# Kernel optimization log

Measured on AMD Instinct MI355X. Metric: run time of the kernel, lower is better.

## Reference

```python
import jax, jax.numpy as jnp
import numpy as np
import math

B, S, D, H = 8, 1024, 512, 8
DH = D // H
SCALE_BASE = 512


def _xpos(x, downscale):
    # x: [B, H, S, DH]; xpos rotary with exponential scale (jamie-stirling RetNet impl)
    s = x.shape[-2]
    d = x.shape[-1]
    half = d // 2
    sv = (jnp.arange(0, d, 2, dtype=jnp.float32) + 0.4 * d) / (1.4 * d)      # [half]
    power = jnp.arange(s, dtype=jnp.float32) / SCALE_BASE
    scale = sv[None, :] ** power[:, None]                                     # [s, half]
    inv_freq = 1.0 / (10000.0 ** (jnp.arange(half, dtype=jnp.float32) / half))
    ang = jnp.arange(s, dtype=jnp.float32)[:, None] * inv_freq[None, :]       # [s, half]
    if downscale:
        scale = 1.0 / scale
    sin = jnp.repeat(jnp.sin(ang) * scale, 2, axis=-1)                        # [s, d]
    cos = jnp.repeat(jnp.cos(ang) * scale, 2, axis=-1)
    rot = jnp.stack((-x[..., 1::2], x[..., ::2]), axis=-1).reshape(x.shape)   # rotate_every_two
    return x * cos + rot * sin


def setup_inputs() -> dict:
    key = jax.random.key(0)
    ks = jax.random.split(key, 7)
    X = jax.random.normal(ks[0], (B, S, D), dtype=jnp.float32)
    # per-head projections stacked: torch init randn/hidden_size
    W_Q = jax.random.normal(ks[1], (H, D, DH), dtype=jnp.float32) / D
    W_K = jax.random.normal(ks[2], (H, D, DH), dtype=jnp.float32) / D
    W_V = jax.random.normal(ks[3], (H, D, DH), dtype=jnp.float32) / D
    W_G = jax.random.normal(ks[4], (D, D), dtype=jnp.float32) / D
    W_O = jax.random.normal(ks[5], (D, D), dtype=jnp.float32) / D
    gn_weight = jnp.ones((D,), dtype=jnp.float32)
    gn_bias = jnp.zeros((D,), dtype=jnp.float32)
    return {"X": X, "W_Q": W_Q, "W_K": W_K, "W_V": W_V, "W_G": W_G,
            "W_O": W_O, "gn_weight": gn_weight, "gn_bias": gn_bias}


def reference(X, W_Q, W_K, W_V, W_G, W_O, gn_weight, gn_bias):
    b, s, _ = X.shape
    # per-head decay gammas and symmetric (non-causal) decay matrix D
    gammas = 1.0 - jnp.exp(jnp.linspace(math.log(1.0 / 32), math.log(1.0 / 512), H)).astype(jnp.float32)
    n = jnp.arange(s)
    Dmat = gammas[:, None, None] ** jnp.abs(n[:, None] - n[None, :]).astype(jnp.float32)  # [H,s,s]
    Q = _xpos(jnp.einsum('bsd,hde->bhse', X, W_Q), False)
    K = _xpos(jnp.einsum('bsd,hde->bhse', X, W_K), True)
    V = jnp.einsum('bsd,hde->bhse', X, W_V)
    scores = jnp.einsum('bhse,bhte->bhst', Q, K)
    p = jax.nn.softmax(scores, axis=-1) * Dmat[None]          # decay-weighted softmax
    Y = jnp.einsum('bhst,bhte->bhse', p, V)                    # [b,H,s,DH]
    Y = jnp.moveaxis(Y, 1, 2).reshape(b, s, H * DH)            # concat heads -> [b,s,D]
    # GroupNorm(H groups) over flattened rows [b*s, D]
    Yg = Y.reshape(-1, H, DH)
    mu = Yg.mean(axis=-1, keepdims=True)
    var = Yg.var(axis=-1, keepdims=True)
    Yn = ((Yg - mu) * jax.lax.rsqrt(var + 1e-5)).reshape(-1, H * DH)
    Yn = (Yn * gn_weight + gn_bias).reshape(b, s, H * DH)
    G = X @ W_G
    swish = G * jax.nn.sigmoid(G)
    return (swish * Yn) @ W_O
```

## Files before the change

### kernel.cpp

```cpp
#include <hip/hip_runtime.h>
#include <math.h>

#define B_ 8
#define S_ 1024
#define D_ 512
#define H_ 8
#define DH_ 64
#define M_ (B_*S_)

typedef __attribute__((ext_vector_type(8))) short short8;
typedef __attribute__((ext_vector_type(4))) short s16x4;
typedef __attribute__((ext_vector_type(4))) float f32x4;

__device__ inline unsigned short bf16h(float x) {
  unsigned u = __float_as_uint(x);
  return (unsigned short)((u + 0x7FFFu + ((u >> 16) & 1u)) >> 16);
}
__device__ inline void tsplit(float x, short& hs, short& ls) {
  unsigned u = __float_as_uint(x);
  hs = (short)(u >> 16);
  float r = x - __uint_as_float(u & 0xFFFF0000u);
  ls = (short)(__float_as_uint(r) >> 16);
}
__device__ inline f32x4 mfma16(short8 a, short8 b, f32x4 c) {
  return __builtin_amdgcn_mfma_f32_16x16x32_bf16(a, b, c, 0, 0, 0);
}

__global__ void xpos_table_kernel(float* __restrict__ tab) {
  int idx = blockIdx.x * 256 + threadIdx.x;
  int s = idx >> 5, i = idx & 31;
  float sv = (2.0f * (float)i + 0.4f * 64.0f) / (1.4f * 64.0f);
  float p = (float)s / 512.0f;
  float scale = powf(sv, p);
  float inv_freq = powf(10000.0f, -((float)i / 32.0f));
  float ang = (float)s * inv_freq;
  float sn = sinf(ang), cs = cosf(ang);
  tab[idx]          = cs * scale;
  tab[32768 + idx]  = sn * scale;
  tab[65536 + idx]  = cs / scale;
  tab[98304 + idx]  = sn / scale;
}

__global__ __launch_bounds__(256) void wprep_kernel(
    const float* __restrict__ Wq, const float* __restrict__ Wk,
    const float* __restrict__ Wv, const float* __restrict__ Wg,
    short* __restrict__ BTh, short* __restrict__ BTl, int gonly) {
  __shared__ float t[64][65];
  const int n0 = blockIdx.x * 64, k0 = blockIdx.y * 64;
  const int tid = threadIdx.x;
  const float* src;
  int ld;
  if (gonly) {
    src = Wg + (size_t)k0 * 512 + n0; ld = 512;
  } else {
    int w = n0 >> 9, nn = n0 & 511;
    if (w == 3) { src = Wg + (size_t)k0 * 512 + nn; ld = 512; }
    else {
      const float* W = (w == 0) ? Wq : ((w == 1) ? Wk : Wv);
      int h = nn >> 6;
      src = W + (size_t)h * D_ * DH_ + (size_t)k0 * 64; ld = 64;
    }
  }
#pragma unroll
  for (int i = 0; i < 4; ++i) {
    int idx = tid + i * 256;
    int kk = idx >> 4, nl4 = (idx & 15) * 4;
    float4 v = *(const float4*)(src + (size_t)kk * ld + nl4);
    t[kk][nl4] = v.x; t[kk][nl4 + 1] = v.y; t[kk][nl4 + 2] = v.z; t[kk][nl4 + 3] = v.w;
  }
  __syncthreads();
#pragma unroll
  for (int i = 0; i < 2; ++i) {
    int idx = tid + i * 256;
    int nl = idx >> 3, ck = idx & 7;
    short8 hh, ll;
#pragma unroll
    for (int j = 0; j < 8; ++j) {
      short h_, l_;
      tsplit(t[ck * 8 + j][nl], h_, l_);
      hh[j] = h_; ll[j] = l_;
    }
    size_t off = (size_t)(n0 + nl) * 512 + k0 + ck * 8;
    *(short8*)(BTh + off) = hh;
    *(short8*)(BTl + off) = ll;
  }
}

template<bool PRESPLIT>
__global__ __launch_bounds__(256) void gemm_mfma_kernel(
    const float* __restrict__ Af,
    const short* __restrict__ Ah, const short* __restrict__ Al,
    const short* __restrict__ BTh, const short* __restrict__ BTl,
    const float* __restrict__ tab,
    short* __restrict__ QhO, short* __restrict__ QlO,
    short* __restrict__ KhO, short* __restrict__ KlO,
    short* __restrict__ VhT, short* __restrict__ VlT,
    float* __restrict__ G, int fused) {
  __shared__ __align__(16) short AsH[128][40];
  __shared__ __align__(16) short AsL[128][40];
  __shared__ __align__(16) short BsH[128][40];
  __shared__ __align__(16) short BsL[128][40];
  const int m0 = blockIdx.x * 128, by = blockIdx.y, n0 = by * 128;
  const int tid = threadIdx.x, w = tid >> 6, lane = tid & 63;
  const int lx = lane & 15, quad = lane >> 4;
  const int wr = w >> 1, wc = w & 1;
  f32x4 acc[4][4] = {};
  for (int k0 = 0; k0 < 512; k0 += 32) {
    if constexpr (PRESPLIT) {
#pragma unroll
      for (int i = 0; i < 2; ++i) {
        int idx = tid + i * 256;
        int r = idx >> 2, sg = (idx & 3) * 8;
        *(short8*)&AsH[r][sg] = *(const short8*)(Ah + (size_t)(m0 + r) * 512 + k0 + sg);
        *(short8*)&AsL[r][sg] = *(const short8*)(Al + (size_t)(m0 + r) * 512 + k0 + sg);
      }
    } else {
      int r = tid >> 1, kh = (tid & 1) * 16;
      const float* ap = Af + (size_t)(m0 + r) * 512 + k0 + kh;
#pragma unroll
      for (int j4 = 0; j4 < 4; ++j4) {
        float4 v = *(const float4*)(ap + j4 * 4);
        s16x4 hh, ll;
        short h_, l_;
        tsplit(v.x, h_, l_); hh[0] = h_; ll[0] = l_;
        tsplit(v.y, h_, l_); hh[1] = h_; ll[1] = l_;
        tsplit(v.z, h_, l_); hh[2] = h_; ll[2] = l_;
        tsplit(v.w, h_, l_); hh[3] = h_; ll[3] = l_;
        *(s16x4*)&AsH[r][kh + j4 * 4] = hh;
        *(s16x4*)&AsL[r][kh + j4 * 4] = ll;
      }
    }
#pragma unroll
    for (int i = 0; i < 2; ++i) {
      int idx = tid + i * 256;
      int r = idx >> 2, sg = (idx & 3) * 8;
      *(short8*)&BsH[r][sg] = *(const short8*)(BTh + (size_t)(n0 + r) * 512 + k0 + sg);
      *(short8*)&BsL[r][sg] = *(const short8*)(BTl + (size_t)(n0 + r) * 512 + k0 + sg);
    }
    __syncthreads();
    short8 fah[4], fal[4], fbh[4], fbl[4];
#pragma unroll
    for (int i = 0; i < 4; ++i) {
      fah[i] = *(const short8*)&AsH[wr * 64 + i * 16 + lx][quad * 8];
      fal[i] = *(const short8*)&AsL[wr * 64 + i * 16 + lx][quad * 8];
      fbh[i] = *(const short8*)&BsH[wc * 64 + i * 16 + lx][quad * 8];
      fbl[i] = *(const short8*)&BsL[wc * 64 + i * 16 + lx][quad * 8];
    }
#pragma unroll
    for (int ms = 0; ms < 4; ++ms)
#pragma unroll
      for (int ns = 0; ns < 4; ++ns) {
        f32x4 a = acc[ms][ns];
        a = mfma16(fah[ms], fbh[ns], a);
        a = mfma16(fal[ms], fbh[ns], a);
        a = mfma16(fah[ms], fbl[ns], a);
        acc[ms][ns] = a;
      }
    __syncthreads();
  }
  if (fused) {
    const int w4 = by >> 2;
    const int ncb = (by & 3) * 128 + wc * 64;
    if (w4 < 2) {
      short* Ph = (w4 == 0) ? QhO : KhO;
      short* Pl = (w4 == 0) ? QlO : KlO;
      const float* ct = tab + (w4 ? 65536 : 0);
      const float* st = tab + (w4 ? 98304 : 32768);
#pragma unroll
      for (int ms = 0; ms < 4; ++ms) {
        const int m = m0 + wr * 64 + ms * 16 + quad * 4;
        const int b = m >> 10, sbase = m & 1023;
#pragma unroll
        for (int ns = 0; ns < 4; ++ns) {
          const int n = ncb + ns * 16 + lx;
          const int h = n >> 6, e = n & 63;
          const int i0 = e >> 1;
          const float sgn = (e & 1) ? 1.0f : -1.0f;
          short* ph = Ph + (((size_t)(b * 8 + h)) * 1024 + sbase) * 64 + e;
          short* pl = Pl + (((size_t)(b * 8 + h)) * 1024 + sbase) * 64 + e;
#pragma unroll
          for (int rg = 0; rg < 4; ++rg) {
            const int s = sbase + rg;
            float v = acc[ms][ns][rg];
            float vp = __shfl_xor(v, 1);
            float o = v * ct[s * 32 + i0] + sgn * vp * st[s * 32 + i0];
            short h_, l_;
            tsplit(o, h_, l_);
            ph[rg * 64] = h_;
            pl[rg * 64] = l_;
          }
        }
      }
    } else if (w4 == 2) {
#pragma unroll
      for (int ms = 0; ms < 4; ++ms) {
        const int m = m0 + wr * 64 + ms * 16 + quad * 4;
        const int b = m >> 10, s = m & 1023;
#pragma unroll
        for (int ns = 0; ns < 4; ++ns) {
          const int n = ncb + ns * 16 + lx;
          const int h = n >> 6, e = n & 63;
          s16x4 hh, ll;
#pragma unroll
          for (int rg = 0; rg < 4; ++rg) {
            short h_, l_;
            tsplit(acc[ms][ns][rg], h_, l_);
            hh[rg] = h_; ll[rg] = l_;
          }
          size_t off = (((size_t)(b * 8 + h)) * 64 + e) * 1024 + s;
          *(s16x4*)(VhT + off) = hh;
          *(s16x4*)(VlT + off) = ll;
        }
      }
    } else {
#pragma unroll
      for (int ms = 0; ms < 4; ++ms) {
        const int m = m0 + wr * 64 + ms * 16 + quad * 4;
#pragma unroll
        for (int ns = 0; ns < 4; ++ns) {
          const int n = ncb + ns * 16 + lx;
#pragma unroll
          for (int rg = 0; rg < 4; ++rg) G[(size_t)(m + rg) * 512 + n] = acc[ms][ns][rg];
        }
      }
    }
  } else {
#pragma unroll
    for (int ms = 0; ms < 4; ++ms) {
      const int m = m0 + wr * 64 + ms * 16 + quad * 4;
#pragma unroll
      for (int ns = 0; ns < 4; ++ns) {
        const int n = n0 + wc * 64 + ns * 16 + lx;
#pragma unroll
        for (int rg = 0; rg < 4; ++rg) G[(size_t)(m + rg) * 512 + n] = acc[ms][ns][rg];
      }
    }
  }
}

__global__ __launch_bounds__(256, 2) void attn_mfma_kernel(
    const short* __restrict__ Qh, const short* __restrict__ Ql,
    const short* __restrict__ Kh, const short* __restrict__ Kl,
    const short* __restrict__ VhT, const short* __restrict__ VlT,
    float* __restrict__ Y) {
  __shared__ __align__(16) short KhS[64][72];
  __shared__ __align__(16) short KlS[64][72];
  __shared__ __align__(16) short VhS[64][72];
  __shared__ __align__(16) short VlS[64][72];
  __shared__ __align__(16) short PhS[4][32][72];
  const int bh = blockIdx.x, s0 = blockIdx.y * 128;
  const int b = bh >> 3, h = bh & 7;
  const int tid = threadIdx.x;
  const int w = tid >> 6, lane = tid & 63;
  const int lx = lane & 15, quad = lane >> 4;
  const int s0w = s0 + w * 32;
  const float l0c = -3.4657359027997265f;
  const float l1c = -6.2383246250395075f;
  const float gamma = 1.0f - expf(l0c + (float)h * (l1c - l0c) / 7.0f);
  const float lg2g = log2f(gamma);
  const short* Qbh = Qh + (size_t)bh * S_ * DH_;
  const short* Qbl = Ql + (size_t)bh * S_ * DH_;
  const short* Kbh = Kh + (size_t)bh * S_ * DH_;
  const short* Kbl = Kl + (size_t)bh * S_ * DH_;
  const short* VbH = VhT + (size_t)bh * DH_ * S_;
  const short* VbL = VlT + (size_t)bh * DH_ * S_;

  float cl[4], cr[4];
#pragma unroll
  for (int ns = 0; ns < 4; ++ns) {
    cl[ns] = exp2f(lg2g * (float)(ns * 16 + lx));
    cr[ns] = exp2f(lg2g * (float)(63 - ns * 16 - lx));
  }

  short8 qfh[2][2], qfl[2][2];
#pragma unroll
  for (int ms = 0; ms < 2; ++ms)
#pragma unroll
    for (int kc = 0; kc < 2; ++kc) {
      size_t off = (size_t)(s0w + ms * 16 + lx) * DH_ + kc * 32 + quad * 8;
      qfh[ms][kc] = *(const short8*)(Qbh + off);
      qfl[ms][kc] = *(const short8*)(Qbl + off);
    }

  f32x4 O[2][4] = {};
  float lsum[2][4] = {};

  for (int t0 = 0; t0 < S_; t0 += 64) {
    __syncthreads();
#pragma unroll
    for (int i = 0; i < 2; ++i) {
      int slot = tid + i * 256;
      int r = slot >> 3, c8 = (slot & 7) * 8;
      *(short8*)&KhS[r][c8] = *(const short8*)(Kbh + (size_t)(t0 + r) * DH_ + c8);
      *(short8*)&KlS[r][c8] = *(const short8*)(Kbl + (size_t)(t0 + r) * DH_ + c8);
      *(short8*)&VhS[r][c8] = *(const short8*)(VbH + (size_t)r * S_ + t0 + c8);
      *(short8*)&VlS[r][c8] = *(const short8*)(VbL + (size_t)r * S_ + t0 + c8);
    }
    __syncthreads();
    f32x4 acc[2][4];
#pragma unroll
    for (int ns = 0; ns < 4; ++ns) {
      short8 kh0 = *(const short8*)&KhS[ns * 16 + lx][quad * 8];
      short8 kh1 = *(const short8*)&KhS[ns * 16 + lx][32 + quad * 8];
      short8 kl0 = *(const short8*)&KlS[ns * 16 + lx][quad * 8];
      short8 kl1 = *(const short8*)&KlS[ns * 16 + lx][32 + quad * 8];
#pragma unroll
      for (int ms = 0; ms < 2; ++ms) {
        f32x4 a = {};
        a = mfma16(qfh[ms][0], kh0, a);
        a = mfma16(qfl[ms][0], kh0, a);
        a = mfma16(qfh[ms][0], kl0, a);
        a = mfma16(qfh[ms][1], kh1, a);
        a = mfma16(qfl[ms][1], kh1, a);
        a = mfma16(qfh[ms][1], kl1, a);
        acc[ms][ns] = a;
      }
    }
    const int cse = (t0 + 63 < s0w) ? 0 : ((t0 > s0w + 31) ? 1 : 2);
#pragma unroll
    for (int ms = 0; ms < 2; ++ms)
#pragma unroll
      for (int rg = 0; rg < 4; ++rg) {
        const int rloc = ms * 16 + quad * 4 + rg;
        const int srow = s0w + rloc;
        float pe[4], p[4];
#pragma unroll
        for (int ns = 0; ns < 4; ++ns) pe[ns] = __expf(acc[ms][ns][rg]);
        lsum[ms][rg] += (pe[0] + pe[1]) + (pe[2] + pe[3]);
        if (cse == 0) {
          float rf = exp2f(lg2g * (float)(srow - t0 - 63));
#pragma unroll
          for (int ns = 0; ns < 4; ++ns) p[ns] = pe[ns] * rf * cr[ns];
        } else if (cse == 1) {
          float rf = exp2f(lg2g * (float)(t0 - srow));
#pragma unroll
          for (int ns = 0; ns < 4; ++ns) p[ns] = pe[ns] * rf * cl[ns];
        } else {
#pragma unroll
          for (int ns = 0; ns < 4; ++ns)
            p[ns] = pe[ns] * exp2f(lg2g * fabsf((float)(srow - (t0 + ns * 16 + lx))));
        }
#pragma unroll
        for (int ns = 0; ns < 4; ++ns)
          PhS[w][rloc][ns * 16 + lx] = (short)bf16h(p[ns]);
      }
    short8 pf[2][2];
#pragma unroll
    for (int ms = 0; ms < 2; ++ms)
#pragma unroll
      for (int kc = 0; kc < 2; ++kc)
        pf[ms][kc] = *(const short8*)&PhS[w][ms * 16 + lx][kc * 32 + quad * 8];
#pragma unroll
    for (int ns = 0; ns < 4; ++ns) {
      short8 vh0 = *(const short8*)&VhS[ns * 16 + lx][quad * 8];
      short8 vh1 = *(const short8*)&VhS[ns * 16 + lx][32 + quad * 8];
      short8 vl0 = *(const short8*)&VlS[ns * 16 + lx][quad * 8];
      short8 vl1 = *(const short8*)&VlS[ns * 16 + lx][32 + quad * 8];
#pragma unroll
      for (int ms = 0; ms < 2; ++ms) {
        f32x4 o = O[ms][ns];
        o = mfma16(pf[ms][0], vh0, o);
        o = mfma16(pf[ms][0], vl0, o);
        o = mfma16(pf[ms][1], vh1, o);
        o = mfma16(pf[ms][1], vl1, o);
        O[ms][ns] = o;
      }
    }
  }
#pragma unroll
  for (int ms = 0; ms < 2; ++ms)
#pragma unroll
    for (int rg = 0; rg < 4; ++rg) {
      float s = lsum[ms][rg];
      s += __shfl_xor(s, 1);
      s += __shfl_xor(s, 2);
      s += __shfl_xor(s, 4);
      s += __shfl_xor(s, 8);
      const float inv = 1.0f / s;
      const int srow = s0w + ms * 16 + quad * 4 + rg;
#pragma unroll
      for (int ns = 0; ns < 4; ++ns)
        Y[((size_t)(b * S_ + srow)) * D_ + h * DH_ + ns * 16 + lx] = O[ms][ns][rg] * inv;
    }
}

__global__ __launch_bounds__(256) void gn_gate_kernel(const float* __restrict__ Y,
                                                      const float* __restrict__ G,
                                                      const float* __restrict__ gnw,
                                                      const float* __restrict__ gnb,
                                                      short* __restrict__ Zh,
                                                      short* __restrict__ Zl) {
  const int r0 = blockIdx.x * 64, h = blockIdx.y, d0 = h * DH_;
  const int tid = threadIdx.x, tx = tid & 15, tyq = tid >> 4;
  float4 wv = *(const float4*)(gnw + d0 + tx * 4);
  float4 bv = *(const float4*)(gnb + d0 + tx * 4);
  float w4[4] = {wv.x, wv.y, wv.z, wv.w};
  float b4[4] = {bv.x, bv.y, bv.z, bv.w};
#pragma unroll
  for (int i = 0; i < 4; ++i) {
    int r = r0 + tyq + i * 16;
    float4 yv = *(const float4*)(Y + (size_t)r * D_ + d0 + tx * 4);
    float y[4] = {yv.x, yv.y, yv.z, yv.w};
    float s = y[0] + y[1] + y[2] + y[3];
    s += __shfl_xor(s, 1); s += __shfl_xor(s, 2); s += __shfl_xor(s, 4); s += __shfl_xor(s, 8);
    const float mu = s * (1.0f / 64.0f);
    float d0_ = y[0] - mu, d1 = y[1] - mu, d2 = y[2] - mu, d3 = y[3] - mu;
    float ss = d0_ * d0_ + d1 * d1 + d2 * d2 + d3 * d3;
    ss += __shfl_xor(ss, 1); ss += __shfl_xor(ss, 2); ss += __shfl_xor(ss, 4); ss += __shfl_xor(ss, 8);
    const float rstd = 1.0f / sqrtf(ss * (1.0f / 64.0f) + 1e-5f);
    float4 gv = *(const float4*)(G + (size_t)r * D_ + d0 + tx * 4);
    float g[4] = {gv.x, gv.y, gv.z, gv.w};
    s16x4 hh, ll;
#pragma unroll
    for (int j = 0; j < 4; ++j) {
      float yn = (y[j] - mu) * rstd * w4[j] + b4[j];
      float sw = g[j] / (1.0f + expf(-g[j]));
      short h_, l_;
      tsplit(sw * yn, h_, l_);
      hh[j] = h_; ll[j] = l_;
    }
    size_t off = (size_t)r * 512 + d0 + tx * 4;
    *(s16x4*)(Zh + off) = hh;
    *(s16x4*)(Zl + off) = ll;
  }
}

extern "C" void kernel_launch(void* const* d_in, const int* in_sizes, int n_in,
                              void* d_out, int out_size, void* d_ws, size_t ws_size,
                              hipStream_t stream) {
  const float* X   = (const float*)d_in[0];
  const float* Wq  = (const float*)d_in[1];
  const float* Wk  = (const float*)d_in[2];
  const float* Wv  = (const float*)d_in[3];
  const float* Wg  = (const float*)d_in[4];
  const float* Wo  = (const float*)d_in[5];
  const float* gnw = (const float*)d_in[6];
  const float* gnb = (const float*)d_in[7];
  float* out = (float*)d_out;
  float* ws  = (float*)d_ws;
  const size_t NB = (size_t)M_ * D_;
  float* R0 = ws;
  float* R1 = ws + NB;
  float* R2 = ws + 2 * NB;
  float* R3 = ws + 3 * NB;
  float* tab = ws + 4 * NB;
  short* BTh = (short*)R3;
  short* BTl = BTh + (size_t)2048 * 512;
  short* Qh = (short*)R0;  short* Ql = Qh + NB;
  short* Kh = (short*)R1;  short* Kl = Kh + NB;
  short* VhT = (short*)R2; short* VlT = VhT + NB;
  float* Yb = R3;
  short* Zh = (short*)R0;  short* Zl = Zh + NB;
  short* BToh = (short*)R1;
  short* BTol = BToh + (size_t)512 * 512;

  wprep_kernel<<<dim3(32, 8), 256, 0, stream>>>(Wq, Wk, Wv, Wg, BTh, BTl, 0);
  xpos_table_kernel<<<128, 256, 0, stream>>>(tab);
  gemm_mfma_kernel<false><<<dim3(64, 16), 256, 0, stream>>>(
      X, nullptr, nullptr, BTh, BTl, tab, Qh, Ql, Kh, Kl, VhT, VlT, out, 1);
  attn_mfma_kernel<<<dim3(64, 8), 256, 0, stream>>>(Qh, Ql, Kh, Kl, VhT, VlT, Yb);
  gn_gate_kernel<<<dim3(128, 8), 256, 0, stream>>>(Yb, out, gnw, gnb, Zh, Zl);
  wprep_kernel<<<dim3(8, 8), 256, 0, stream>>>(nullptr, nullptr, nullptr, Wo, BToh, BTol, 1);
  gemm_mfma_kernel<true><<<dim3(64, 4), 256, 0, stream>>>(
      nullptr, Zh, Zl, BToh, BTol, nullptr, nullptr, nullptr, nullptr, nullptr,
      nullptr, nullptr, out, 0);
}
```

Before: 241.9 us.

## Fuse GroupNorm and swish gate into attention epilogue, restage GEMM A operand

Moves the GroupNorm, swish gating and hi/lo bf16 split into the attention kernel's epilogue. This drops the separate gn_gate kernel and the fp32 Y round-trip through global memory. The projection GEMM now stages A as fp32 in shared memory and splits it when loading fragments, and the output GEMM reads its pre-split A straight from global memory, skipping LDS. It also swaps the round-to-nearest-even bf16 rounding of P for a cheaper round-half-up, which can change numerics slightly, and the direct global A reads may be less coalesced.

```diff
diff --git a/kernel.cpp b/kernel.cpp
--- a/kernel.cpp
+++ b/kernel.cpp
@@ -12,10 +12,6 @@
 typedef __attribute__((ext_vector_type(4))) short s16x4;
 typedef __attribute__((ext_vector_type(4))) float f32x4;
 
-__device__ inline unsigned short bf16h(float x) {
-  unsigned u = __float_as_uint(x);
-  return (unsigned short)((u + 0x7FFFu + ((u >> 16) & 1u)) >> 16);
-}
 __device__ inline void tsplit(float x, short& hs, short& ls) {
   unsigned u = __float_as_uint(x);
   hs = (short)(u >> 16);
@@ -86,7 +82,7 @@
   }
 }
 
-template<bool PRESPLIT>
+template<int AMODE>
 __global__ __launch_bounds__(256) void gemm_mfma_kernel(
     const float* __restrict__ Af,
     const short* __restrict__ Ah, const short* __restrict__ Al,
@@ -96,8 +92,7 @@
     short* __restrict__ KhO, short* __restrict__ KlO,
     short* __restrict__ VhT, short* __restrict__ VlT,
     float* __restrict__ G, int fused) {
-  __shared__ __align__(16) short AsH[128][40];
-  __shared__ __align__(16) short AsL[128][40];
+  __shared__ __align__(16) float AsF[AMODE == 0 ? 128 : 1][36];
   __shared__ __align__(16) short BsH[128][40];
   __shared__ __align__(16) short BsL[128][40];
   const int m0 = blockIdx.x * 128, by = blockIdx.y, n0 = by * 128;
@@ -106,29 +101,12 @@
   const int wr = w >> 1, wc = w & 1;
   f32x4 acc[4][4] = {};
   for (int k0 = 0; k0 < 512; k0 += 32) {
-    if constexpr (PRESPLIT) {
-#pragma unroll
-      for (int i = 0; i < 2; ++i) {
-        int idx = tid + i * 256;
-        int r = idx >> 2, sg = (idx & 3) * 8;
-        *(short8*)&AsH[r][sg] = *(const short8*)(Ah + (size_t)(m0 + r) * 512 + k0 + sg);
-        *(short8*)&AsL[r][sg] = *(const short8*)(Al + (size_t)(m0 + r) * 512 + k0 + sg);
-      }
-    } else {
-      int r = tid >> 1, kh = (tid & 1) * 16;
-      const float* ap = Af + (size_t)(m0 + r) * 512 + k0 + kh;
-#pragma unroll
-      for (int j4 = 0; j4 < 4; ++j4) {
-        float4 v = *(const float4*)(ap + j4 * 4);
-        s16x4 hh, ll;
-        short h_, l_;
-        tsplit(v.x, h_, l_); hh[0] = h_; ll[0] = l_;
-        tsplit(v.y, h_, l_); hh[1] = h_; ll[1] = l_;
-        tsplit(v.z, h_, l_); hh[2] = h_; ll[2] = l_;
-        tsplit(v.w, h_, l_); hh[3] = h_; ll[3] = l_;
-        *(s16x4*)&AsH[r][kh + j4 * 4] = hh;
-        *(s16x4*)&AsL[r][kh + j4 * 4] = ll;
-      }
+    if constexpr (AMODE == 0) {
+      int r = tid >> 1, cb = (tid & 1) * 16;
+      const float* ap = Af + (size_t)(m0 + r) * 512 + k0 + cb;
+#pragma unroll
+      for (int j4 = 0; j4 < 4; ++j4)
+        *(float4*)&AsF[r][cb + j4 * 4] = *(const float4*)(ap + j4 * 4);
     }
 #pragma unroll
     for (int i = 0; i < 2; ++i) {
@@ -141,8 +119,23 @@
     short8 fah[4], fal[4], fbh[4], fbl[4];
 #pragma unroll
     for (int i = 0; i < 4; ++i) {
-      fah[i] = *(const short8*)&AsH[wr * 64 + i * 16 + lx][quad * 8];
-      fal[i] = *(const short8*)&AsL[wr * 64 + i * 16 + lx][quad * 8];
+      if constexpr (AMODE == 0) {
+        const float* ap2 = &AsF[wr * 64 + i * 16 + lx][quad * 8];
+        float4 a = *(const float4*)ap2, c = *(const float4*)(ap2 + 4);
+        float xs[8] = {a.x, a.y, a.z, a.w, c.x, c.y, c.z, c.w};
+        short8 hh, ll;
+#pragma unroll
+        for (int j = 0; j < 8; ++j) {
+          short h_, l_;
+          tsplit(xs[j], h_, l_);
+          hh[j] = h_; ll[j] = l_;
+        }
+        fah[i] = hh; fal[i] = ll;
+      } else {
+        size_t aoff = (size_t)(m0 + wr * 64 + i * 16 + lx) * 512 + k0 + quad * 8;
+        fah[i] = *(const short8*)(Ah + aoff);
+        fal[i] = *(const short8*)(Al + aoff);
+      }
       fbh[i] = *(const short8*)&BsH[wc * 64 + i * 16 + lx][quad * 8];
       fbl[i] = *(const short8*)&BsL[wc * 64 + i * 16 + lx][quad * 8];
     }
@@ -242,7 +235,9 @@
     const short* __restrict__ Qh, const short* __restrict__ Ql,
     const short* __restrict__ Kh, const short* __restrict__ Kl,
     const short* __restrict__ VhT, const short* __restrict__ VlT,
-    float* __restrict__ Y) {
+    const float* __restrict__ Gp,
+    const float* __restrict__ gnw, const float* __restrict__ gnb,
+    short* __restrict__ Zh, short* __restrict__ Zl) {
   __shared__ __align__(16) short KhS[64][72];
   __shared__ __align__(16) short KlS[64][72];
   __shared__ __align__(16) short VhS[64][72];
@@ -265,11 +260,13 @@
   const short* VbH = VhT + (size_t)bh * DH_ * S_;
   const short* VbL = VlT + (size_t)bh * DH_ * S_;
 
-  float cl[4], cr[4];
+  float cl[4], cr[4], w4g[4], b4g[4];
 #pragma unroll
   for (int ns = 0; ns < 4; ++ns) {
     cl[ns] = exp2f(lg2g * (float)(ns * 16 + lx));
     cr[ns] = exp2f(lg2g * (float)(63 - ns * 16 - lx));
+    w4g[ns] = gnw[h * DH_ + ns * 16 + lx];
+    b4g[ns] = gnb[h * DH_ + ns * 16 + lx];
   }
 
   short8 qfh[2][2], qfl[2][2];
@@ -342,7 +339,7 @@
         }
 #pragma unroll
         for (int ns = 0; ns < 4; ++ns)
-          PhS[w][rloc][ns * 16 + lx] = (short)bf16h(p[ns]);
+          PhS[w][rloc][ns * 16 + lx] = (short)((__float_as_uint(p[ns]) + 0x8000u) >> 16);
       }
     short8 pf[2][2];
 #pragma unroll
@@ -378,51 +375,35 @@
       s += __shfl_xor(s, 8);
       const float inv = 1.0f / s;
       const int srow = s0w + ms * 16 + quad * 4 + rg;
-#pragma unroll
-      for (int ns = 0; ns < 4; ++ns)
-        Y[((size_t)(b * S_ + srow)) * D_ + h * DH_ + ns * 16 + lx] = O[ms][ns][rg] * inv;
-    }
-}
-
-__global__ __launch_bounds__(256) void gn_gate_kernel(const float* __restrict__ Y,
-                                                      const float* __restrict__ G,
-                                                      const float* __restrict__ gnw,
-                                                      const float* __restrict__ gnb,
-                                                      short* __restrict__ Zh,
-                                                      short* __restrict__ Zl) {
-  const int r0 = blockIdx.x * 64, h = blockIdx.y, d0 = h * DH_;
-  const int tid = threadIdx.x, tx = tid & 15, tyq = tid >> 4;
-  float4 wv = *(const float4*)(gnw + d0 + tx * 4);
-  float4 bv = *(const float4*)(gnb + d0 + tx * 4);
-  float w4[4] = {wv.x, wv.y, wv.z, wv.w};
-  float b4[4] = {bv.x, bv.y, bv.z, bv.w};
-#pragma unroll
-  for (int i = 0; i < 4; ++i) {
-    int r = r0 + tyq + i * 16;
-    float4 yv = *(const float4*)(Y + (size_t)r * D_ + d0 + tx * 4);
-    float y[4] = {yv.x, yv.y, yv.z, yv.w};
-    float s = y[0] + y[1] + y[2] + y[3];
-    s += __shfl_xor(s, 1); s += __shfl_xor(s, 2); s += __shfl_xor(s, 4); s += __shfl_xor(s, 8);
-    const float mu = s * (1.0f / 64.0f);
-    float d0_ = y[0] - mu, d1 = y[1] - mu, d2 = y[2] - mu, d3 = y[3] - mu;
-    float ss = d0_ * d0_ + d1 * d1 + d2 * d2 + d3 * d3;
-    ss += __shfl_xor(ss, 1); ss += __shfl_xor(ss, 2); ss += __shfl_xor(ss, 4); ss += __shfl_xor(ss, 8);
-    const float rstd = 1.0f / sqrtf(ss * (1.0f / 64.0f) + 1e-5f);
-    float4 gv = *(const float4*)(G + (size_t)r * D_ + d0 + tx * 4);
-    float g[4] = {gv.x, gv.y, gv.z, gv.w};
-    s16x4 hh, ll;
-#pragma unroll
-    for (int j = 0; j < 4; ++j) {
-      float yn = (y[j] - mu) * rstd * w4[j] + b4[j];
-      float sw = g[j] / (1.0f + expf(-g[j]));
-      short h_, l_;
-      tsplit(sw * yn, h_, l_);
-      hh[j] = h_; ll[j] = l_;
-    }
-    size_t off = (size_t)r * 512 + d0 + tx * 4;
-    *(s16x4*)(Zh + off) = hh;
-    *(s16x4*)(Zl + off) = ll;
-  }
+      float y[4];
+      float rs = 0.0f;
+#pragma unroll
+      for (int ns = 0; ns < 4; ++ns) { y[ns] = O[ms][ns][rg] * inv; rs += y[ns]; }
+      rs += __shfl_xor(rs, 1);
+      rs += __shfl_xor(rs, 2);
+      rs += __shfl_xor(rs, 4);
+      rs += __shfl_xor(rs, 8);
+      const float mu = rs * (1.0f / 64.0f);
+      float vv = 0.0f;
+#pragma unroll
+      for (int ns = 0; ns < 4; ++ns) { float d = y[ns] - mu; vv += d * d; }
+      vv += __shfl_xor(vv, 1);
+      vv += __shfl_xor(vv, 2);
+      vv += __shfl_xor(vv, 4);
+      vv += __shfl_xor(vv, 8);
+      const float rstd = rsqrtf(vv * (1.0f / 64.0f) + 1e-5f);
+      const size_t base = (size_t)(b * S_ + srow) * D_ + h * DH_;
+#pragma unroll
+      for (int ns = 0; ns < 4; ++ns) {
+        float g = Gp[base + ns * 16 + lx];
+        float sw = g / (1.0f + __expf(-g));
+        float z = sw * ((y[ns] - mu) * rstd * w4g[ns] + b4g[ns]);
+        short zh_, zl_;
+        tsplit(z, zh_, zl_);
+        Zh[base + ns * 16 + lx] = zh_;
+        Zl[base + ns * 16 + lx] = zl_;
+      }
+    }
 }
 
 extern "C" void kernel_launch(void* const* d_in, const int* in_sizes, int n_in,
@@ -449,19 +430,18 @@
   short* Qh = (short*)R0;  short* Ql = Qh + NB;
   short* Kh = (short*)R1;  short* Kl = Kh + NB;
   short* VhT = (short*)R2; short* VlT = VhT + NB;
-  float* Yb = R3;
-  short* Zh = (short*)R0;  short* Zl = Zh + NB;
+  short* Zh = (short*)R3;  short* Zl = Zh + NB;
   short* BToh = (short*)R1;
   short* BTol = BToh + (size_t)512 * 512;
 
   wprep_kernel<<<dim3(32, 8), 256, 0, stream>>>(Wq, Wk, Wv, Wg, BTh, BTl, 0);
   xpos_table_kernel<<<128, 256, 0, stream>>>(tab);
-  gemm_mfma_kernel<false><<<dim3(64, 16), 256, 0, stream>>>(
+  gemm_mfma_kernel<0><<<dim3(64, 16), 256, 0, stream>>>(
       X, nullptr, nullptr, BTh, BTl, tab, Qh, Ql, Kh, Kl, VhT, VlT, out, 1);
-  attn_mfma_kernel<<<dim3(64, 8), 256, 0, stream>>>(Qh, Ql, Kh, Kl, VhT, VlT, Yb);
-  gn_gate_kernel<<<dim3(128, 8), 256, 0, stream>>>(Yb, out, gnw, gnb, Zh, Zl);
+  attn_mfma_kernel<<<dim3(64, 8), 256, 0, stream>>>(
+      Qh, Ql, Kh, Kl, VhT, VlT, out, gnw, gnb, Zh, Zl);
   wprep_kernel<<<dim3(8, 8), 256, 0, stream>>>(nullptr, nullptr, nullptr, Wo, BToh, BTol, 1);
-  gemm_mfma_kernel<true><<<dim3(64, 4), 256, 0, stream>>>(
+  gemm_mfma_kernel<1><<<dim3(64, 4), 256, 0, stream>>>(
       nullptr, Zh, Zl, BToh, BTol, nullptr, nullptr, nullptr, nullptr, nullptr,
       nullptr, nullptr, out, 0);
 }
```

New measurement: 243.7 us. About the same (+0.7%).
